# Kernel optimization log

Measured on AMD Instinct MI355X. Metric: run time of the kernel, lower is better.

## Reference

```python
import jax, jax.numpy as jnp
import numpy as np

B, NQ, NN, EMB, H, D = 64, 256, 512, 128, 8, 16
SQRT_EMB = float(np.sqrt(EMB))
LOGIT_CLIP = 10.0


def setup_inputs() -> dict:
    key = jax.random.key(0)
    ks = jax.random.split(key, 9)
    encoded_last_node = jax.random.normal(ks[0], (B, NQ, EMB), jnp.float32)
    attr = jax.random.uniform(ks[1], (B, NQ, 1), jnp.float32)  # e.g. remaining load in [0,1]
    encoded_nodes = jax.random.normal(ks[2], (B, NN, EMB), jnp.float32)
    ninf_mask = jnp.where(jax.random.uniform(ks[3], (B, NQ, NN)) < 0.15,
                          -jnp.inf, 0.0).astype(jnp.float32)
    def lin(k, fan_in, fan_out):
        lim = 1.0 / np.sqrt(fan_in)
        return jax.random.uniform(k, (fan_in, fan_out), jnp.float32, -lim, lim)
    Wq_last = lin(ks[4], EMB + 1, H * D)
    Wk = lin(ks[5], EMB, H * D)
    Wv = lin(ks[6], EMB, H * D)
    Wcomb = lin(ks[7], H * D, EMB)
    bcomb = jax.random.uniform(ks[8], (EMB,), jnp.float32, -1.0 / np.sqrt(H * D), 1.0 / np.sqrt(H * D))
    return dict(encoded_last_node=encoded_last_node, attr=attr,
                encoded_nodes=encoded_nodes, ninf_mask=ninf_mask,
                Wq_last=Wq_last, Wk=Wk, Wv=Wv, Wcomb=Wcomb, bcomb=bcomb)


def _heads(x):  # [B, T, H*D] -> [B, H, T, D]
    return x.reshape(x.shape[0], x.shape[1], H, D).transpose(0, 2, 1, 3)


def reference(encoded_last_node, attr, encoded_nodes, ninf_mask,
              Wq_last, Wk, Wv, Wcomb, bcomb):
    # fix fully-masked rows: un-mask index 0 (matches torch mask_inf patch)
    all_inf = jnp.isinf(ninf_mask).all(axis=2)  # [B, NQ]
    ninf_mask = ninf_mask.at[:, :, 0].set(jnp.where(all_inf, 0.0, ninf_mask[:, :, 0]))

    # set_kv
    k = _heads(encoded_nodes @ Wk)  # [B,H,NN,D]
    v = _heads(encoded_nodes @ Wv)  # [B,H,NN,D]

    # q from last node + attr
    q = _heads(jnp.concatenate([encoded_last_node, attr], axis=2) @ Wq_last)  # [B,H,NQ,D]

    # masked multi-head attention
    score = jnp.einsum('bhnd,bhmd->bhnm', q, k) / jnp.sqrt(jnp.float32(D))
    score = score + ninf_mask[:, None, :, :]          # rank3 mask broadcast over heads
    weights = jax.nn.softmax(score, axis=-1)          # [B,H,NQ,NN]
    out = jnp.einsum('bhnm,bhmd->bhnd', weights, v)
    out_concat = out.transpose(0, 2, 1, 3).reshape(B, NQ, H * D)
    mh_atten_out = out_concat @ Wcomb + bcomb         # [B,NQ,EMB]

    # single-head compatibility score + tanh clip + mask + softmax
    score2 = jnp.einsum('bne,bme->bnm', mh_atten_out, encoded_nodes) / SQRT_EMB
    logits = LOGIT_CLIP * jnp.tanh(score2) + ninf_mask
    probs = jax.nn.softmax(logits, axis=2)            # [B,NQ,NN]
    return probs
```

## Files before the change

kernel.cpp:

```cpp
#include <hip/hip_runtime.h>
#include <math.h>

#define NB    64
#define NQn   256
#define NNn   512
#define HDn   128
#define LOG2E 1.44269504088896340736f
#define INV_SQRT_EMB 0.08838834764831845f

__device__ __forceinline__ float4 ldg4(const float* p) {
    return *reinterpret_cast<const float4*>(p);
}

__global__ __launch_bounds__(256, 4)
void mask_transpose(const float* __restrict__ mask, unsigned char* __restrict__ maskT8)
{
    const int tid = threadIdx.x;
    const int w   = tid >> 6;
    const int n   = blockIdx.z * 64 + (tid & 63);
    const int b   = blockIdx.x;
    const int q0  = blockIdx.y * 64 + w * 16;
    unsigned int u[4] = {0u, 0u, 0u, 0u};
    #pragma unroll
    for (int j = 0; j < 16; ++j) {
        float v = mask[((size_t)(b * NQn + q0 + j)) * NNn + n];
        unsigned int bit = (v != 0.0f) ? 1u : 0u;
        u[j >> 2] |= bit << (8 * (j & 3));
    }
    *reinterpret_cast<uint4*>(maskT8 + ((size_t)(b * NNn + n)) * NQn + q0) =
        make_uint4(u[0], u[1], u[2], u[3]);
}

__global__ __launch_bounds__(256, 2)
void proj_kernel(const float* __restrict__ X,
                 const float* __restrict__ W0, const float* __restrict__ W1,
                 const float* __restrict__ wrow, const float* __restrict__ attr,
                 const float* __restrict__ bias,
                 float* __restrict__ Y0, float* __restrict__ Y1)
{
    __shared__ float Xs[64 * 128];
    __shared__ float Wt[64 * 128];
    const int tid = threadIdx.x;
    const int rg = tid >> 4;
    const int cg = tid & 15;
    const int rowblk = blockIdx.x * 64;
    const int colbase = blockIdx.y * 64;

    #pragma unroll
    for (int i = 0; i < 8; ++i) {
        int idx = tid + 256 * i;
        int r = idx >> 5;
        int c4 = idx & 31;
        float4 v = ldg4(X + (rowblk + r) * 128 + c4 * 4);
        *reinterpret_cast<float4*>(&Xs[r * 128 + ((c4 ^ (r & 7)) << 2)]) = v;
    }

    for (int pass = 0; pass < 2; ++pass) {
        if (pass && (W1 == nullptr)) break;
        const float* W = pass ? W1 : W0;
        float* Y = pass ? Y1 : Y0;
        __syncthreads();
        #pragma unroll
        for (int i = 0; i < 32; ++i) {
            int idx = tid + 256 * i;
            int k = idx >> 6;
            int c = idx & 63;
            float w = W[k * 128 + colbase + c];
            Wt[c * 128 + ((((k >> 2) ^ (c & 7)) << 2) | (k & 3))] = w;
        }
        __syncthreads();

        float acc[4][4];
        #pragma unroll
        for (int r = 0; r < 4; ++r)
            #pragma unroll
            for (int c = 0; c < 4; ++c) acc[r][c] = 0.f;

        const int rsw = rg & 7;
        const int csw = cg & 7;
        #pragma unroll 8
        for (int k4 = 0; k4 < 32; ++k4) {
            float4 a[4], bv[4];
            #pragma unroll
            for (int r = 0; r < 4; ++r)
                a[r] = *reinterpret_cast<const float4*>(&Xs[(rg + 16 * r) * 128 + ((k4 ^ rsw) << 2)]);
            #pragma unroll
            for (int c = 0; c < 4; ++c)
                bv[c] = *reinterpret_cast<const float4*>(&Wt[(cg + 16 * c) * 128 + ((k4 ^ csw) << 2)]);
            #pragma unroll
            for (int r = 0; r < 4; ++r)
                #pragma unroll
                for (int c = 0; c < 4; ++c)
                    acc[r][c] += a[r].x * bv[c].x + a[r].y * bv[c].y
                               + a[r].z * bv[c].z + a[r].w * bv[c].w;
        }

        if (attr != nullptr) {
            #pragma unroll
            for (int r = 0; r < 4; ++r) {
                float av = attr[rowblk + rg + 16 * r];
                #pragma unroll
                for (int c = 0; c < 4; ++c)
                    acc[r][c] += av * wrow[colbase + cg + 16 * c];
            }
        }
        #pragma unroll
        for (int r = 0; r < 4; ++r) {
            int row = rowblk + rg + 16 * r;
            #pragma unroll
            for (int c = 0; c < 4; ++c) {
                int col = colbase + cg + 16 * c;
                float o = acc[r][c];
                if (bias != nullptr) o += bias[col];
                Y[row * 128 + col] = o;
            }
        }
    }
}

__global__ __launch_bounds__(512, 2)
void attn_kernel(const float* __restrict__ Q, const float* __restrict__ K,
                 const float* __restrict__ V, const unsigned int* __restrict__ maskTu,
                 float* __restrict__ P0, float* __restrict__ P1,
                 float* __restrict__ P2, float* __restrict__ P3,
                 float* __restrict__ L0, float* __restrict__ L1,
                 float* __restrict__ L2, float* __restrict__ L3)
{
    __shared__ float Ks[32 * 128];
    __shared__ float Vs[32 * 128];
    const int tid  = threadIdx.x;
    const int lane = tid & 63;
    const int h    = tid >> 6;
    const int b    = blockIdx.x;
    const int ns   = blockIdx.y;
    const int nbase = ns * 128;

    float qv[4][16];
    {
        const float sc = 0.25f * LOG2E;
        #pragma unroll
        for (int qq = 0; qq < 4; ++qq) {
            const float* qp = Q + ((size_t)(b * NQn + 4 * lane + qq)) * 128 + h * 16;
            #pragma unroll
            for (int j = 0; j < 4; ++j) {
                float4 tv = ldg4(qp + 4 * j);
                qv[qq][4 * j + 0] = tv.x * sc;
                qv[qq][4 * j + 1] = tv.y * sc;
                qv[qq][4 * j + 2] = tv.z * sc;
                qv[qq][4 * j + 3] = tv.w * sc;
            }
        }
    }

    float out[4][16];
    #pragma unroll
    for (int qq = 0; qq < 4; ++qq)
        #pragma unroll
        for (int d = 0; d < 16; ++d) out[qq][d] = 0.f;
    float ls[4] = {0.f, 0.f, 0.f, 0.f};

    const unsigned int* mbase = maskTu + (((size_t)(b * NNn + nbase) * NQn) >> 2) + lane;

    for (int t = 0; t < 4; ++t) {
        __syncthreads();
        {
            const float* kg = K + ((size_t)(b * NNn + nbase + t * 32)) * 128;
            const float* vg = V + ((size_t)(b * NNn + nbase + t * 32)) * 128;
            float4 k0 = ldg4(kg + tid * 4);
            float4 k1 = ldg4(kg + (tid + 512) * 4);
            float4 v0 = ldg4(vg + tid * 4);
            float4 v1 = ldg4(vg + (tid + 512) * 4);
            *reinterpret_cast<float4*>(&Ks[tid * 4]) = k0;
            *reinterpret_cast<float4*>(&Ks[(tid + 512) * 4]) = k1;
            *reinterpret_cast<float4*>(&Vs[tid * 4]) = v0;
            *reinterpret_cast<float4*>(&Vs[(tid + 512) * 4]) = v1;
        }
        __syncthreads();

        const float* kbase = &Ks[h * 16];
        const float* vbase = &Vs[h * 16];
        for (int n = 0; n < 32; ++n) {
            const float* kr = kbase + n * 128;
            const float* vr = vbase + n * 128;
            float kf[16], vf[16];
            *reinterpret_cast<float4*>(&kf[0])  = *reinterpret_cast<const float4*>(kr);
            *reinterpret_cast<float4*>(&kf[4])  = *reinterpret_cast<const float4*>(kr + 4);
            *reinterpret_cast<float4*>(&kf[8])  = *reinterpret_cast<const float4*>(kr + 8);
            *reinterpret_cast<float4*>(&kf[12]) = *reinterpret_cast<const float4*>(kr + 12);
            *reinterpret_cast<float4*>(&vf[0])  = *reinterpret_cast<const float4*>(vr);
            *reinterpret_cast<float4*>(&vf[4])  = *reinterpret_cast<const float4*>(vr + 4);
            *reinterpret_cast<float4*>(&vf[8])  = *reinterpret_cast<const float4*>(vr + 8);
            *reinterpret_cast<float4*>(&vf[12]) = *reinterpret_cast<const float4*>(vr + 12);
            unsigned int m4 = mbase[(t * 32 + n) * (NQn / 4)];

            float p[4];
            #pragma unroll
            for (int qq = 0; qq < 4; ++qq) {
                float aP = qv[qq][0]*kf[0] + qv[qq][1]*kf[1] + qv[qq][2]*kf[2] + qv[qq][3]*kf[3];
                float aQ = qv[qq][4]*kf[4] + qv[qq][5]*kf[5] + qv[qq][6]*kf[6] + qv[qq][7]*kf[7];
                float aR = qv[qq][8]*kf[8] + qv[qq][9]*kf[9] + qv[qq][10]*kf[10] + qv[qq][11]*kf[11];
                float aS = qv[qq][12]*kf[12] + qv[qq][13]*kf[13] + qv[qq][14]*kf[14] + qv[qq][15]*kf[15];
                p[qq] = __builtin_amdgcn_exp2f((aP + aQ) + (aR + aS));
            }
            p[0] = (m4 & 0x000000ffu) ? 0.f : p[0];
            p[1] = (m4 & 0x0000ff00u) ? 0.f : p[1];
            p[2] = (m4 & 0x00ff0000u) ? 0.f : p[2];
            p[3] = (m4 & 0xff000000u) ? 0.f : p[3];
            ls[0] += p[0]; ls[1] += p[1]; ls[2] += p[2]; ls[3] += p[3];
            #pragma unroll
            for (int d = 0; d < 16; ++d) {
                out[0][d] += p[0] * vf[d];
                out[1][d] += p[1] * vf[d];
                out[2][d] += p[2] * vf[d];
                out[3][d] += p[3] * vf[d];
            }
        }
    }

    float* P = (ns == 0) ? P0 : (ns == 1) ? P1 : (ns == 2) ? P2 : P3;
    float* L = (ns == 0) ? L0 : (ns == 1) ? L1 : (ns == 2) ? L2 : L3;
    #pragma unroll
    for (int qq = 0; qq < 4; ++qq) {
        float* op = P + ((size_t)(b * NQn + 4 * lane + qq)) * 128 + h * 16;
        *reinterpret_cast<float4*>(op)      = make_float4(out[qq][0],  out[qq][1],  out[qq][2],  out[qq][3]);
        *reinterpret_cast<float4*>(op + 4)  = make_float4(out[qq][4],  out[qq][5],  out[qq][6],  out[qq][7]);
        *reinterpret_cast<float4*>(op + 8)  = make_float4(out[qq][8],  out[qq][9],  out[qq][10], out[qq][11]);
        *reinterpret_cast<float4*>(op + 12) = make_float4(out[qq][12], out[qq][13], out[qq][14], out[qq][15]);
        L[(b * NQn + 4 * lane + qq) * 8 + h] = ls[qq];
    }
}

__global__ __launch_bounds__(256, 2)
void proj_comb_kernel(const float* __restrict__ P0, const float* __restrict__ P1,
                      const float* __restrict__ P2, const float* __restrict__ P3,
                      const float* __restrict__ L0, const float* __restrict__ L1,
                      const float* __restrict__ L2, const float* __restrict__ L3,
                      const float* __restrict__ V,
                      const float* __restrict__ W0, const float* __restrict__ bias,
                      float* __restrict__ Y0)
{
    __shared__ float Xs[64 * 128];
    __shared__ float Wt[64 * 128];
    const int tid = threadIdx.x;
    const int rg = tid >> 4;
    const int cg = tid & 15;
    const int rowblk = blockIdx.x * 64;
    const int colbase = blockIdx.y * 64;

    #pragma unroll
    for (int i = 0; i < 8; ++i) {
        int idx = tid + 256 * i;
        int r = idx >> 5;
        int c4 = idx & 31;
        int row = rowblk + r;
        int hh = c4 >> 2;
        float l = (L0[row * 8 + hh] + L1[row * 8 + hh])
                + (L2[row * 8 + hh] + L3[row * 8 + hh]);
        float4 v;
        if (l == 0.0f) {
            v = ldg4(V + ((size_t)(row >> 8)) * NNn * 128 + c4 * 4);
        } else {
            float4 a = ldg4(P0 + (size_t)row * 128 + c4 * 4);
            float4 c = ldg4(P1 + (size_t)row * 128 + c4 * 4);
            float4 d = ldg4(P2 + (size_t)row * 128 + c4 * 4);
            float4 e = ldg4(P3 + (size_t)row * 128 + c4 * 4);
            float inv = __builtin_amdgcn_rcpf(l);
            v = make_float4((a.x + c.x + d.x + e.x) * inv,
                            (a.y + c.y + d.y + e.y) * inv,
                            (a.z + c.z + d.z + e.z) * inv,
                            (a.w + c.w + d.w + e.w) * inv);
        }
        *reinterpret_cast<float4*>(&Xs[r * 128 + ((c4 ^ (r & 7)) << 2)]) = v;
    }

    __syncthreads();
    #pragma unroll
    for (int i = 0; i < 32; ++i) {
        int idx = tid + 256 * i;
        int k = idx >> 6;
        int c = idx & 63;
        float w = W0[k * 128 + colbase + c];
        Wt[c * 128 + ((((k >> 2) ^ (c & 7)) << 2) | (k & 3))] = w;
    }
    __syncthreads();

    float acc[4][4];
    #pragma unroll
    for (int r = 0; r < 4; ++r)
        #pragma unroll
        for (int c = 0; c < 4; ++c) acc[r][c] = 0.f;

    const int rsw = rg & 7;
    const int csw = cg & 7;
    #pragma unroll 8
    for (int k4 = 0; k4 < 32; ++k4) {
        float4 a[4], bv[4];
        #pragma unroll
        for (int r = 0; r < 4; ++r)
            a[r] = *reinterpret_cast<const float4*>(&Xs[(rg + 16 * r) * 128 + ((k4 ^ rsw) << 2)]);
        #pragma unroll
        for (int c = 0; c < 4; ++c)
            bv[c] = *reinterpret_cast<const float4*>(&Wt[(cg + 16 * c) * 128 + ((k4 ^ csw) << 2)]);
        #pragma unroll
        for (int r = 0; r < 4; ++r)
            #pragma unroll
            for (int c = 0; c < 4; ++c)
                acc[r][c] += a[r].x * bv[c].x + a[r].y * bv[c].y
                           + a[r].z * bv[c].z + a[r].w * bv[c].w;
    }

    #pragma unroll
    for (int r = 0; r < 4; ++r) {
        int row = rowblk + rg + 16 * r;
        #pragma unroll
        for (int c = 0; c < 4; ++c) {
            int col = colbase + cg + 16 * c;
            Y0[row * 128 + col] = acc[r][c] + bias[col];
        }
    }
}

__global__ __launch_bounds__(512, 2)
void final_kernel(const float* __restrict__ MH, const float* __restrict__ EN,
                  const float* __restrict__ mask, float* __restrict__ OUT)
{
    __shared__ float ENs[128 * 128];
    const int tid = threadIdx.x;
    const int qg = tid >> 4;
    const int mg = tid & 15;
    const int b  = blockIdx.x >> 2;
    const int q0 = (blockIdx.x & 3) * 64;

    const float* mhbase = MH + (b * NQn + q0) * 128;
    float pr[2][32];
    float psum[2] = {0.f, 0.f};
    const int msw = mg & 7;

    #pragma unroll
    for (int t = 0; t < 4; ++t) {
        const int m0 = t * 128;
        __syncthreads();
        #pragma unroll
        for (int i = 0; i < 8; ++i) {
            int idx = tid + 512 * i;
            int r = idx >> 5;
            int c4 = idx & 31;
            float4 v = ldg4(EN + (b * NNn + m0 + r) * 128 + c4 * 4);
            *reinterpret_cast<float4*>(&ENs[r * 128 + ((c4 ^ (r & 7)) << 2)]) = v;
        }
        __syncthreads();

        float acc[2][8];
        #pragma unroll
        for (int qq = 0; qq < 2; ++qq)
            #pragma unroll
            for (int c = 0; c < 8; ++c) acc[qq][c] = 0.f;

        #pragma unroll 4
        for (int k4 = 0; k4 < 32; ++k4) {
            float4 a0 = ldg4(mhbase + (qg * 2 + 0) * 128 + k4 * 4);
            float4 a1 = ldg4(mhbase + (qg * 2 + 1) * 128 + k4 * 4);
            float4 bv[8];
            #pragma unroll
            for (int c = 0; c < 8; ++c)
                bv[c] = *reinterpret_cast<const float4*>(&ENs[(mg + 16 * c) * 128 + ((k4 ^ msw) << 2)]);
            #pragma unroll
            for (int c = 0; c < 8; ++c) {
                acc[0][c] += a0.x*bv[c].x + a0.y*bv[c].y + a0.z*bv[c].z + a0.w*bv[c].w;
                acc[1][c] += a1.x*bv[c].x + a1.y*bv[c].y + a1.z*bv[c].z + a1.w*bv[c].w;
            }
        }

        #pragma unroll
        for (int qq = 0; qq < 2; ++qq) {
            const int q = q0 + qg * 2 + qq;
            const float* mrow = mask + (b * NQn + q) * NNn + m0;
            #pragma unroll
            for (int c = 0; c < 8; ++c) {
                int m = mg + 16 * c;
                float s2 = acc[qq][c] * INV_SQRT_EMB;
                float e  = __builtin_amdgcn_exp2f(s2 * (2.0f * LOG2E));
                float rc = __builtin_amdgcn_rcpf(e + 1.0f);
                float mv = mrow[m];
                float pv = __builtin_amdgcn_exp2f((mv - 20.0f * rc) * LOG2E);
                pr[qq][t * 8 + c] = pv;
                psum[qq] += pv;
            }
        }
    }

    #pragma unroll
    for (int qq = 0; qq < 2; ++qq) {
        float s = psum[qq];
        s += __shfl_xor(s, 1);
        s += __shfl_xor(s, 2);
        s += __shfl_xor(s, 4);
        s += __shfl_xor(s, 8);
        psum[qq] = s;
    }

    #pragma unroll
    for (int qq = 0; qq < 2; ++qq) {
        const int q = q0 + qg * 2 + qq;
        float* orow = OUT + (b * NQn + q) * NNn;
        if (psum[qq] == 0.0f) {
            #pragma unroll
            for (int t = 0; t < 4; ++t)
                #pragma unroll
                for (int c = 0; c < 8; ++c) {
                    int m = t * 128 + mg + 16 * c;
                    orow[m] = (m == 0) ? 1.0f : 0.0f;
                }
        } else {
            float inv = __builtin_amdgcn_rcpf(psum[qq]);
            #pragma unroll
            for (int t = 0; t < 4; ++t)
                #pragma unroll
                for (int c = 0; c < 8; ++c)
                    orow[t * 128 + mg + 16 * c] = pr[qq][t * 8 + c] * inv;
        }
    }
}

extern "C" void kernel_launch(void* const* d_in, const int* in_sizes, int n_in,
                              void* d_out, int out_size, void* d_ws, size_t ws_size,
                              hipStream_t stream) {
    const float* enc_last  = (const float*)d_in[0];
    const float* attr      = (const float*)d_in[1];
    const float* enc_nodes = (const float*)d_in[2];
    const float* mask      = (const float*)d_in[3];
    const float* Wq        = (const float*)d_in[4];
    const float* Wk        = (const float*)d_in[5];
    const float* Wv        = (const float*)d_in[6];
    const float* Wcomb     = (const float*)d_in[7];
    const float* bcomb     = (const float*)d_in[8];
    float* out = (float*)d_out;

    float* Kbuf = (float*)d_ws;
    float* Vbuf = Kbuf + (size_t)NB * NNn * 128;
    float* Qbuf = Vbuf + (size_t)NB * NNn * 128;
    float* P0   = Qbuf + (size_t)NB * NQn * 128;
    float* P1   = P0   + (size_t)NB * NQn * 128;
    float* P2   = P1   + (size_t)NB * NQn * 128;
    float* P3   = P2   + (size_t)NB * NQn * 128;
    float* L0   = P3   + (size_t)NB * NQn * 128;
    float* L1   = L0   + (size_t)NB * NQn * 8;
    float* L2   = L1   + (size_t)NB * NQn * 8;
    float* L3   = L2   + (size_t)NB * NQn * 8;
    unsigned char* maskT8 = (unsigned char*)(L3 + (size_t)NB * NQn * 8);
    float* MH   = Qbuf;

    mask_transpose<<<dim3(NB, NQn / 64, NNn / 64), 256, 0, stream>>>(mask, maskT8);
    proj_kernel<<<dim3(NB * NNn / 64, 2), 256, 0, stream>>>(
        enc_nodes, Wk, Wv, nullptr, nullptr, nullptr, Kbuf, Vbuf);
    proj_kernel<<<dim3(NB * NQn / 64, 2), 256, 0, stream>>>(
        enc_last, Wq, nullptr, Wq + 128 * 128, attr, nullptr, Qbuf, nullptr);
    attn_kernel<<<dim3(NB, 4), 512, 0, stream>>>(
        Qbuf, Kbuf, Vbuf, (const unsigned int*)maskT8,
        P0, P1, P2, P3, L0, L1, L2, L3);
    proj_comb_kernel<<<dim3(NB * NQn / 64, 2), 256, 0, stream>>>(
        P0, P1, P2, P3, L0, L1, L2, L3, Vbuf, Wcomb, bcomb, MH);
    final_kernel<<<dim3(NB * NQn / 64), 512, 0, stream>>>(
        MH, enc_nodes, mask, out);
}
```

Before: 230.2 us.

## Retile mask transpose, split attention heads across blocks, prefetch K/V, halve final tile

The mask transpose now stages a 64x64 tile through padded shared memory, so both the global reads and the byte-packed writes are coalesced. The attention kernel moves from 512 to 256 threads with heads split over a new grid z dimension, doubling the block count, and it prefetches the next K/V tile into registers while computing the current one. The final kernel gives each thread one query row instead of two and launches twice as many blocks with a higher occupancy hint. Each block still loads its full K/V and EN tiles, so the extra blocks add redundant loads in exchange for more parallelism and latency hiding.

```diff
diff --git a/kernel.cpp b/kernel.cpp
--- a/kernel.cpp
+++ b/kernel.cpp
@@ -15,19 +15,31 @@
 __global__ __launch_bounds__(256, 4)
 void mask_transpose(const float* __restrict__ mask, unsigned char* __restrict__ maskT8)
 {
+    __shared__ float Ms[64 * 65];
     const int tid = threadIdx.x;
-    const int w   = tid >> 6;
-    const int n   = blockIdx.z * 64 + (tid & 63);
     const int b   = blockIdx.x;
-    const int q0  = blockIdx.y * 64 + w * 16;
+    const int q0  = blockIdx.y * 64;
+    const int n0  = blockIdx.z * 64;
+    const int qg  = tid >> 6;
+    const int ln  = tid & 63;
+
+    #pragma unroll
+    for (int j = 0; j < 16; ++j) {
+        int q = qg * 16 + j;
+        Ms[q * 65 + ln] = mask[((size_t)(b * NQn + q0 + q)) * NNn + n0 + ln];
+    }
+    __syncthreads();
+
+    const int n  = tid >> 2;
+    const int qc = (tid & 3) * 16;
     unsigned int u[4] = {0u, 0u, 0u, 0u};
     #pragma unroll
     for (int j = 0; j < 16; ++j) {
-        float v = mask[((size_t)(b * NQn + q0 + j)) * NNn + n];
+        float v = Ms[(qc + j) * 65 + n];
         unsigned int bit = (v != 0.0f) ? 1u : 0u;
         u[j >> 2] |= bit << (8 * (j & 3));
     }
-    *reinterpret_cast<uint4*>(maskT8 + ((size_t)(b * NNn + n)) * NQn + q0) =
+    *reinterpret_cast<uint4*>(maskT8 + ((size_t)(b * NNn + n0 + n)) * NQn + q0 + qc) =
         make_uint4(u[0], u[1], u[2], u[3]);
 }
 
@@ -118,7 +130,7 @@
     }
 }
 
-__global__ __launch_bounds__(512, 2)
+__global__ __launch_bounds__(256, 2)
 void attn_kernel(const float* __restrict__ Q, const float* __restrict__ K,
                  const float* __restrict__ V, const unsigned int* __restrict__ maskTu,
                  float* __restrict__ P0, float* __restrict__ P1,
@@ -130,7 +142,7 @@
     __shared__ float Vs[32 * 128];
     const int tid  = threadIdx.x;
     const int lane = tid & 63;
-    const int h    = tid >> 6;
+    const int h    = blockIdx.z * 4 + (tid >> 6);
     const int b    = blockIdx.x;
     const int ns   = blockIdx.y;
     const int nbase = ns * 128;
@@ -161,21 +173,33 @@
 
     const unsigned int* mbase = maskTu + (((size_t)(b * NNn + nbase) * NQn) >> 2) + lane;
 
+    const float* kg = K + ((size_t)(b * NNn + nbase)) * 128;
+    const float* vg = V + ((size_t)(b * NNn + nbase)) * 128;
+
+    float4 krp[4], vrp[4];
+    #pragma unroll
+    for (int i = 0; i < 4; ++i) {
+        krp[i] = ldg4(kg + (tid + 256 * i) * 4);
+        vrp[i] = ldg4(vg + (tid + 256 * i) * 4);
+    }
+
     for (int t = 0; t < 4; ++t) {
         __syncthreads();
-        {
-            const float* kg = K + ((size_t)(b * NNn + nbase + t * 32)) * 128;
-            const float* vg = V + ((size_t)(b * NNn + nbase + t * 32)) * 128;
-            float4 k0 = ldg4(kg + tid * 4);
-            float4 k1 = ldg4(kg + (tid + 512) * 4);
-            float4 v0 = ldg4(vg + tid * 4);
-            float4 v1 = ldg4(vg + (tid + 512) * 4);
-            *reinterpret_cast<float4*>(&Ks[tid * 4]) = k0;
-            *reinterpret_cast<float4*>(&Ks[(tid + 512) * 4]) = k1;
-            *reinterpret_cast<float4*>(&Vs[tid * 4]) = v0;
-            *reinterpret_cast<float4*>(&Vs[(tid + 512) * 4]) = v1;
-        }
-        __syncthreads();
+        #pragma unroll
+        for (int i = 0; i < 4; ++i) {
+            *reinterpret_cast<float4*>(&Ks[(tid + 256 * i) * 4]) = krp[i];
+            *reinterpret_cast<float4*>(&Vs[(tid + 256 * i) * 4]) = vrp[i];
+        }
+        __syncthreads();
+        if (t < 3) {
+            const float* kg2 = kg + (t + 1) * 32 * 128;
+            const float* vg2 = vg + (t + 1) * 32 * 128;
+            #pragma unroll
+            for (int i = 0; i < 4; ++i) {
+                krp[i] = ldg4(kg2 + (tid + 256 * i) * 4);
+                vrp[i] = ldg4(vg2 + (tid + 256 * i) * 4);
+            }
+        }
 
         const float* kbase = &Ks[h * 16];
         const float* vbase = &Vs[h * 16];
@@ -320,7 +344,7 @@
     }
 }
 
-__global__ __launch_bounds__(512, 2)
+__global__ __launch_bounds__(512, 4)
 void final_kernel(const float* __restrict__ MH, const float* __restrict__ EN,
                   const float* __restrict__ mask, float* __restrict__ OUT)
 {
@@ -328,12 +352,12 @@
     const int tid = threadIdx.x;
     const int qg = tid >> 4;
     const int mg = tid & 15;
-    const int b  = blockIdx.x >> 2;
-    const int q0 = (blockIdx.x & 3) * 64;
-
-    const float* mhbase = MH + (b * NQn + q0) * 128;
-    float pr[2][32];
-    float psum[2] = {0.f, 0.f};
+    const int b  = blockIdx.x >> 3;
+    const int q0 = (blockIdx.x & 7) * 32;
+
+    const float* mhrow = MH + (b * NQn + q0 + qg) * 128;
+    float pr[32];
+    float psum = 0.f;
     const int msw = mg & 7;
 
     #pragma unroll
@@ -350,75 +374,61 @@
         }
         __syncthreads();
 
-        float acc[2][8];
-        #pragma unroll
-        for (int qq = 0; qq < 2; ++qq)
-            #pragma unroll
-            for (int c = 0; c < 8; ++c) acc[qq][c] = 0.f;
+        float acc[8];
+        #pragma unroll
+        for (int c = 0; c < 8; ++c) acc[c] = 0.f;
 
         #pragma unroll 4
         for (int k4 = 0; k4 < 32; ++k4) {
-            float4 a0 = ldg4(mhbase + (qg * 2 + 0) * 128 + k4 * 4);
-            float4 a1 = ldg4(mhbase + (qg * 2 + 1) * 128 + k4 * 4);
+            float4 a0 = ldg4(mhrow + k4 * 4);
             float4 bv[8];
             #pragma unroll
             for (int c = 0; c < 8; ++c)
                 bv[c] = *reinterpret_cast<const float4*>(&ENs[(mg + 16 * c) * 128 + ((k4 ^ msw) << 2)]);
             #pragma unroll
-            for (int c = 0; c < 8; ++c) {
-                acc[0][c] += a0.x*bv[c].x + a0.y*bv[c].y + a0.z*bv[c].z + a0.w*bv[c].w;
-                acc[1][c] += a1.x*bv[c].x + a1.y*bv[c].y + a1.z*bv[c].z + a1.w*bv[c].w;
-            }
-        }
-
-        #pragma unroll
-        for (int qq = 0; qq < 2; ++qq) {
-            const int q = q0 + qg * 2 + qq;
-            const float* mrow = mask + (b * NQn + q) * NNn + m0;
-            #pragma unroll
-            for (int c = 0; c < 8; ++c) {
-                int m = mg + 16 * c;
-                float s2 = acc[qq][c] * INV_SQRT_EMB;
-                float e  = __builtin_amdgcn_exp2f(s2 * (2.0f * LOG2E));
-                float rc = __builtin_amdgcn_rcpf(e + 1.0f);
-                float mv = mrow[m];
-                float pv = __builtin_amdgcn_exp2f((mv - 20.0f * rc) * LOG2E);
-                pr[qq][t * 8 + c] = pv;
-                psum[qq] += pv;
-            }
-        }
-    }
-
-    #pragma unroll
-    for (int qq = 0; qq < 2; ++qq) {
-        float s = psum[qq];
+            for (int c = 0; c < 8; ++c)
+                acc[c] += a0.x*bv[c].x + a0.y*bv[c].y + a0.z*bv[c].z + a0.w*bv[c].w;
+        }
+
+        const float* mrow = mask + (b * NQn + q0 + qg) * NNn + m0;
+        #pragma unroll
+        for (int c = 0; c < 8; ++c) {
+            int m = mg + 16 * c;
+            float s2 = acc[c] * INV_SQRT_EMB;
+            float e  = __builtin_amdgcn_exp2f(s2 * (2.0f * LOG2E));
+            float rc = __builtin_amdgcn_rcpf(e + 1.0f);
+            float mv = mrow[m];
+            float pv = __builtin_amdgcn_exp2f((mv - 20.0f * rc) * LOG2E);
+            pr[t * 8 + c] = pv;
+            psum += pv;
+        }
+    }
+
+    {
+        float s = psum;
         s += __shfl_xor(s, 1);
         s += __shfl_xor(s, 2);
         s += __shfl_xor(s, 4);
         s += __shfl_xor(s, 8);
-        psum[qq] = s;
-    }
-
-    #pragma unroll
-    for (int qq = 0; qq < 2; ++qq) {
-        const int q = q0 + qg * 2 + qq;
-        float* orow = OUT + (b * NQn + q) * NNn;
-        if (psum[qq] == 0.0f) {
-            #pragma unroll
-            for (int t = 0; t < 4; ++t)
-                #pragma unroll
-                for (int c = 0; c < 8; ++c) {
-                    int m = t * 128 + mg + 16 * c;
-                    orow[m] = (m == 0) ? 1.0f : 0.0f;
-                }
-        } else {
-            float inv = __builtin_amdgcn_rcpf(psum[qq]);
-            #pragma unroll
-            for (int t = 0; t < 4; ++t)
-                #pragma unroll
-                for (int c = 0; c < 8; ++c)
-                    orow[t * 128 + mg + 16 * c] = pr[qq][t * 8 + c] * inv;
-        }
+        psum = s;
+    }
+
+    float* orow = OUT + (b * NQn + q0 + qg) * NNn;
+    if (psum == 0.0f) {
+        #pragma unroll
+        for (int t = 0; t < 4; ++t)
+            #pragma unroll
+            for (int c = 0; c < 8; ++c) {
+                int m = t * 128 + mg + 16 * c;
+                orow[m] = (m == 0) ? 1.0f : 0.0f;
+            }
+    } else {
+        float inv = __builtin_amdgcn_rcpf(psum);
+        #pragma unroll
+        for (int t = 0; t < 4; ++t)
+            #pragma unroll
+            for (int c = 0; c < 8; ++c)
+                orow[t * 128 + mg + 16 * c] = pr[t * 8 + c] * inv;
     }
 }
 
@@ -455,11 +465,11 @@
         enc_nodes, Wk, Wv, nullptr, nullptr, nullptr, Kbuf, Vbuf);
     proj_kernel<<<dim3(NB * NQn / 64, 2), 256, 0, stream>>>(
         enc_last, Wq, nullptr, Wq + 128 * 128, attr, nullptr, Qbuf, nullptr);
-    attn_kernel<<<dim3(NB, 4), 512, 0, stream>>>(
+    attn_kernel<<<dim3(NB, 4, 2), 256, 0, stream>>>(
         Qbuf, Kbuf, Vbuf, (const unsigned int*)maskT8,
         P0, P1, P2, P3, L0, L1, L2, L3);
     proj_comb_kernel<<<dim3(NB * NQn / 64, 2), 256, 0, stream>>>(
         P0, P1, P2, P3, L0, L1, L2, L3, Vbuf, Wcomb, bcomb, MH);
-    final_kernel<<<dim3(NB * NQn / 64), 512, 0, stream>>>(
+    final_kernel<<<dim3(NB * NQn / 32), 512, 0, stream>>>(
         MH, enc_nodes, mask, out);
 }
```

New measurement: 248.7 us. 1.08x slower.
